# Performance work log

Hardware: AMD Instinct MI355X
Metric: run time of the kernel (lower is better)

## Reference

```python
import jax, jax.numpy as jnp
import numpy as np
from jax import lax

HORIZON = 333.0
LAM = 0.95
DISCOUNT = 1.0 - 1.0 / HORIZON  # contdisc=False

B, T, D, H = 1024, 65, 512, 512


def _mlp(x, W1, b1, W2, b2, W3, b3):
    # x: [B, T, D] -> scalar critic mean per step [B, T]
    h = jax.nn.silu(jnp.einsum('btd,dh->bth', x, W1) + b1)
    h = jax.nn.silu(jnp.einsum('bth,hk->btk', h, W2) + b2)
    out = jnp.einsum('bth,ho->bto', h, W3) + b3
    return out[..., 0]


def setup_inputs() -> dict:
    key = jax.random.key(0)
    ks = jax.random.split(key, 8)
    s = 1.0 / np.sqrt(D)
    sh = 1.0 / np.sqrt(H)
    return {
        'feat': jax.random.normal(ks[0], (B, T, D), jnp.float32),
        'reward': jax.random.normal(ks[1], (B, T), jnp.float32) * 0.1,
        'cont': jnp.ones((B, T), jnp.float32),
        'voffset': jnp.zeros((1,), jnp.float32),
        'vscale': jnp.ones((1,), jnp.float32),
        'W1n': jax.random.normal(ks[2], (D, H), jnp.float32) * s,
        'b1n': jnp.zeros((H,), jnp.float32),
        'W2n': jax.random.normal(ks[3], (H, H), jnp.float32) * sh,
        'b2n': jnp.zeros((H,), jnp.float32),
        'W3n': jax.random.normal(ks[4], (H, 1), jnp.float32) * sh,
        'b3n': jnp.zeros((1,), jnp.float32),
        'W1s': jax.random.normal(ks[5], (D, H), jnp.float32) * s,
        'b1s': jnp.zeros((H,), jnp.float32),
        'W2s': jax.random.normal(ks[6], (H, H), jnp.float32) * sh,
        'b2s': jnp.zeros((H,), jnp.float32),
        'W3s': jax.random.normal(ks[7], (H, 1), jnp.float32) * sh,
        'b3s': jnp.zeros((1,), jnp.float32),
    }


def reference(feat, reward, cont, voffset, vscale,
              W1n, b1n, W2n, b2n, W3n, b3n,
              W1s, b1s, W2s, b2s, W3s, b3s):
    critic = _mlp(feat, W1n, b1n, W2n, b2n, W3n, b3n)        # [B, T]
    slowcritic = _mlp(feat, W1s, b1s, W2s, b2s, W3s, b3s)    # [B, T]
    val = critic * vscale + voffset
    slowval = slowcritic * vscale + voffset
    tarval = slowval  # config.agent.slowtar = True

    disc = cont[:, 1:] * DISCOUNT                             # [B, T-1]
    interm = reward[:, 1:] + (1.0 - LAM) * disc * tarval[:, 1:]
    boot = tarval[:, -1]                                      # [B]

    # reversed linear recurrence r_t = interm_t + disc_t*lam*r_{t+1}
    xs = (jnp.moveaxis(interm, 1, 0), jnp.moveaxis(disc, 1, 0))  # [T-1, B]

    def step(carry, x):
        i_t, d_t = x
        r = i_t + d_t * LAM * carry
        return r, r

    _, ys = lax.scan(step, boot, xs, reverse=True)            # [T-1, B], time order t=0..T-2
    ret = jnp.moveaxis(ys, 0, 1)                              # [B, T-1]
    return ret
```

## Files before the change

### kernel.cpp

```cpp
#include <hip/hip_runtime.h>
#include <stdint.h>


#define MROWS 66560
#define RBLK 520
#define LAMF 0.95f
#define DISCF ((float)(1.0 - 1.0 / 333.0))

typedef __attribute__((ext_vector_type(8))) __bf16 bf16x8;
typedef __attribute__((ext_vector_type(4))) float f32x4;
typedef __attribute__((ext_vector_type(4))) unsigned int u32x4;

__device__ __forceinline__ unsigned short f2bf(float f) {
  unsigned int u = __float_as_uint(f);
  return (unsigned short)((u + 0x7FFFu + ((u >> 16) & 1u)) >> 16);
}
__device__ __forceinline__ float silu_f(float x) { return x / (1.0f + __expf(-x)); }

__device__ __forceinline__ void gload_lds16(const void* g, void* l) {
  __builtin_amdgcn_global_load_lds(
      (const __attribute__((address_space(1))) void*)g,
      (__attribute__((address_space(3))) void*)l, 16, 0, 0);
}

__device__ __forceinline__ u32x4 pack8(const f32x4& a, const f32x4& b) {
  union { unsigned short h[8]; u32x4 u; } p;
  p.h[0] = f2bf(a[0]); p.h[1] = f2bf(a[1]); p.h[2] = f2bf(a[2]); p.h[3] = f2bf(a[3]);
  p.h[4] = f2bf(b[0]); p.h[5] = f2bf(b[1]); p.h[6] = f2bf(b[2]); p.h[7] = f2bf(b[3]);
  return p.u;
}

__global__ __launch_bounds__(256) void prep_kernel(
    const float* __restrict__ W1, const float* __restrict__ W2,
    unsigned short* __restrict__ Wt1, unsigned short* __restrict__ Wt2,
    float* __restrict__ tarval) {
  int b = blockIdx.x;
  if (b < 128) {
    const float* W = (b < 64) ? W1 : W2;
    unsigned short* Wt = (b < 64) ? Wt1 : Wt2;
    int tb = b & 63;
    int tk = (tb >> 3) * 64;
    int tn = (tb & 7) * 64;
    __shared__ float tile[64][65];
    int tx = threadIdx.x & 63;
    int ty4 = threadIdx.x >> 6;
#pragma unroll
    for (int i = 0; i < 16; ++i) {
      int row = ty4 * 16 + i;
      tile[row][tx] = W[(size_t)(tk + row) * 512 + tn + tx];
    }
    __syncthreads();
#pragma unroll
    for (int i = 0; i < 16; ++i) {
      int nrow = ty4 * 16 + i;
      Wt[(size_t)(tn + nrow) * 512 + tk + tx] = f2bf(tile[tx][nrow]);
    }
  } else {
    int id = (b - 128) * 256 + threadIdx.x;
#pragma unroll
    for (int i = 0; i < 17; ++i) {
      int idx = id + i * 4096;
      if (idx < MROWS) tarval[idx] = 0.0f;
    }
  }
}

__device__ __forceinline__ void tile_map(int bid, int& rb, int& cb) {
  int xcd = bid & 7;
  int idx = bid >> 3;
  rb = xcd * 65 + (idx >> 2);
  cb = idx & 3;
}

__global__ __launch_bounds__(256) void gemm1_kernel(
    const float* __restrict__ A, const unsigned short* __restrict__ Bt,
    const float* __restrict__ bias, unsigned short* __restrict__ Hout) {
  __shared__ __align__(16) unsigned char lds[65536];

  int rb, cb; tile_map(blockIdx.x, rb, cb);
  const int m0 = rb * 128, n0 = cb * 128;
  const int tid = threadIdx.x;
  const int lane = tid & 63, w = tid >> 6;
  const int wr = w >> 1, wc = w & 1;
  const int q = lane >> 4, r = lane & 15;
  const unsigned int rx = (unsigned)(r & 7) << 4;

  f32x4 acc[4][4] = {};
  f32x4 pa[8];

  const int a_row_off = tid >> 3;
  const int a_col = (tid & 7) * 8;
  const unsigned int awx = ((unsigned)((tid >> 3) & 7)) << 4;
  const int b_row_off = w * 8 + (lane >> 3);
  const int b_col = ((lane & 7) ^ (lane >> 3)) * 8;

#pragma unroll
  for (int i = 0; i < 4; ++i) {
    const float* s = A + (size_t)(m0 + i * 32 + a_row_off) * 512 + a_col;
    pa[2 * i] = *(const f32x4*)s; pa[2 * i + 1] = *(const f32x4*)(s + 4);
  }
#pragma unroll
  for (int i = 0; i < 4; ++i)
    gload_lds16(Bt + (size_t)(n0 + i * 32 + b_row_off) * 512 + b_col,
                lds + 16384 + i * 4096 + w * 1024);
#pragma unroll
  for (int i = 0; i < 4; ++i)
    gload_lds16(Bt + (size_t)(n0 + i * 32 + b_row_off) * 512 + 64 + b_col,
                lds + 49152 + i * 4096 + w * 1024);
#pragma unroll
  for (int i = 0; i < 4; ++i)
    *(u32x4*)(lds + ((unsigned)(i * 4096 + tid * 16) ^ awx)) =
        pack8(pa[2 * i], pa[2 * i + 1]);

#pragma unroll
  for (int t = 0; t < 8; ++t) {
    if (t < 7) asm volatile("s_waitcnt vmcnt(4) lgkmcnt(0)" ::: "memory");
    else       asm volatile("s_waitcnt vmcnt(0) lgkmcnt(0)" ::: "memory");
    __builtin_amdgcn_s_barrier();

    unsigned char* Acur = lds + (t & 1) * 32768;
    unsigned char* Bcur = Acur + 16384;

    if (t < 7) {
      const int ks = (t + 1) * 64;
#pragma unroll
      for (int i = 0; i < 4; ++i) {
        const float* s = A + (size_t)(m0 + i * 32 + a_row_off) * 512 + ks + a_col;
        pa[2 * i] = *(const f32x4*)s; pa[2 * i + 1] = *(const f32x4*)(s + 4);
      }
    }

    bf16x8 af[2][4], bfr[2][4];
#pragma unroll
    for (int kk = 0; kk < 2; ++kk) {
      const unsigned int kb = kk * 64 + q * 16;
#pragma unroll
      for (int m = 0; m < 4; ++m) {
        const unsigned int row = wr * 64 + m * 16 + r;
        af[kk][m] = *(const bf16x8*)(Acur + ((row * 128 + kb) ^ rx));
      }
#pragma unroll
      for (int n = 0; n < 4; ++n) {
        const unsigned int row = wc * 64 + n * 16 + r;
        bfr[kk][n] = *(const bf16x8*)(Bcur + ((row * 128 + kb) ^ rx));
      }
    }
    asm volatile("s_waitcnt lgkmcnt(0)" ::: "memory");
    __builtin_amdgcn_sched_barrier(0);
    __builtin_amdgcn_s_barrier();

    if (t + 2 < 8) {
      const int ks = (t + 2) * 64;
#pragma unroll
      for (int i = 0; i < 4; ++i)
        gload_lds16(Bt + (size_t)(n0 + i * 32 + b_row_off) * 512 + ks + b_col,
                    Bcur + i * 4096 + w * 1024);
    }
    if (t < 7) {
      unsigned char* Anx = lds + ((t + 1) & 1) * 32768;
#pragma unroll
      for (int i = 0; i < 4; ++i)
        *(u32x4*)(Anx + ((unsigned)(i * 4096 + tid * 16) ^ awx)) =
            pack8(pa[2 * i], pa[2 * i + 1]);
    }

#pragma unroll
    for (int kk = 0; kk < 2; ++kk)
#pragma unroll
      for (int m = 0; m < 4; ++m)
#pragma unroll
        for (int n = 0; n < 4; ++n)
          acc[m][n] = __builtin_amdgcn_mfma_f32_16x16x32_bf16(af[kk][m], bfr[kk][n], acc[m][n], 0, 0, 0);
  }

#pragma unroll
  for (int n = 0; n < 4; ++n) {
    const int col = n0 + wc * 64 + n * 16 + r;
    const float bn = bias[col];
#pragma unroll
    for (int m = 0; m < 4; ++m) {
      const int rbase = m0 + wr * 64 + m * 16 + q * 4;
#pragma unroll
      for (int i = 0; i < 4; ++i)
        Hout[(size_t)(rbase + i) * 512 + col] = f2bf(silu_f(acc[m][n][i] + bn));
    }
  }
}

__global__ __launch_bounds__(256) void gemm2_kernel(
    const unsigned short* __restrict__ A, const unsigned short* __restrict__ Bt,
    const float* __restrict__ bias, const float* __restrict__ W3,
    float* __restrict__ tarval) {
  __shared__ __align__(16) unsigned char lds[65536];

  int rb, cb; tile_map(blockIdx.x, rb, cb);
  const int m0 = rb * 128, n0 = cb * 128;
  const int tid = threadIdx.x;
  const int lane = tid & 63, w = tid >> 6;
  const int wr = w >> 1, wc = w & 1;
  const int q = lane >> 4, r = lane & 15;
  const unsigned int rx = (unsigned)(r & 7) << 4;

  f32x4 acc[4][4] = {};
  const int s_row_off = w * 8 + (lane >> 3);
  const int s_col = ((lane & 7) ^ (lane >> 3)) * 8;

#pragma unroll
  for (int i = 0; i < 4; ++i) {
    gload_lds16(A  + (size_t)(m0 + i * 32 + s_row_off) * 512 + s_col,
                lds + i * 4096 + w * 1024);
    gload_lds16(Bt + (size_t)(n0 + i * 32 + s_row_off) * 512 + s_col,
                lds + 16384 + i * 4096 + w * 1024);
  }
#pragma unroll
  for (int i = 0; i < 4; ++i) {
    gload_lds16(A  + (size_t)(m0 + i * 32 + s_row_off) * 512 + 64 + s_col,
                lds + 32768 + i * 4096 + w * 1024);
    gload_lds16(Bt + (size_t)(n0 + i * 32 + s_row_off) * 512 + 64 + s_col,
                lds + 49152 + i * 4096 + w * 1024);
  }

#pragma unroll
  for (int t = 0; t < 8; ++t) {
    if (t < 7) asm volatile("s_waitcnt vmcnt(8) lgkmcnt(0)" ::: "memory");
    else       asm volatile("s_waitcnt vmcnt(0) lgkmcnt(0)" ::: "memory");
    __builtin_amdgcn_s_barrier();

    unsigned char* Acur = lds + (t & 1) * 32768;
    unsigned char* Bcur = Acur + 16384;

    bf16x8 af[2][4], bfr[2][4];
#pragma unroll
    for (int kk = 0; kk < 2; ++kk) {
      const unsigned int kb = kk * 64 + q * 16;
#pragma unroll
      for (int m = 0; m < 4; ++m) {
        const unsigned int row = wr * 64 + m * 16 + r;
        af[kk][m] = *(const bf16x8*)(Acur + ((row * 128 + kb) ^ rx));
      }
#pragma unroll
      for (int n = 0; n < 4; ++n) {
        const unsigned int row = wc * 64 + n * 16 + r;
        bfr[kk][n] = *(const bf16x8*)(Bcur + ((row * 128 + kb) ^ rx));
      }
    }
    asm volatile("s_waitcnt lgkmcnt(0)" ::: "memory");
    __builtin_amdgcn_sched_barrier(0);
    __builtin_amdgcn_s_barrier();

    if (t + 2 < 8) {
      const int ks = (t + 2) * 64;
#pragma unroll
      for (int i = 0; i < 4; ++i) {
        gload_lds16(A  + (size_t)(m0 + i * 32 + s_row_off) * 512 + ks + s_col,
                    Acur + i * 4096 + w * 1024);
        gload_lds16(Bt + (size_t)(n0 + i * 32 + s_row_off) * 512 + ks + s_col,
                    Bcur + i * 4096 + w * 1024);
      }
    }

#pragma unroll
    for (int kk = 0; kk < 2; ++kk)
#pragma unroll
      for (int m = 0; m < 4; ++m)
#pragma unroll
        for (int n = 0; n < 4; ++n)
          acc[m][n] = __builtin_amdgcn_mfma_f32_16x16x32_bf16(af[kk][m], bfr[kk][n], acc[m][n], 0, 0, 0);
  }

#pragma unroll
  for (int m = 0; m < 4; ++m) {
    float ps0 = 0.f, ps1 = 0.f, ps2 = 0.f, ps3 = 0.f;
#pragma unroll
    for (int n = 0; n < 4; ++n) {
      const int col = n0 + wc * 64 + n * 16 + r;
      const float bn = bias[col];
      const float w3 = W3[col];
      ps0 += silu_f(acc[m][n][0] + bn) * w3;
      ps1 += silu_f(acc[m][n][1] + bn) * w3;
      ps2 += silu_f(acc[m][n][2] + bn) * w3;
      ps3 += silu_f(acc[m][n][3] + bn) * w3;
    }
    float ps[4] = {ps0, ps1, ps2, ps3};
#pragma unroll
    for (int i = 0; i < 4; ++i) {
      float v = ps[i];
      v += __shfl_xor(v, 1);
      v += __shfl_xor(v, 2);
      v += __shfl_xor(v, 4);
      v += __shfl_xor(v, 8);
      if (r == 0) {
        int row = m0 + wr * 64 + m * 16 + q * 4 + i;
        atomicAdd(&tarval[row], v);
      }
    }
  }
}

__global__ __launch_bounds__(64) void scan_kernel(
    const float* __restrict__ tarval, const float* __restrict__ reward,
    const float* __restrict__ cont, const float* __restrict__ voffset,
    const float* __restrict__ vscale, const float* __restrict__ b3,
    float* __restrict__ out) {
  __shared__ float tv[64];
  __shared__ float ret[64];
  const int b = blockIdx.x, t = threadIdx.x;
  tv[t] = (tarval[b * 65 + 1 + t] + b3[0]) * vscale[0] + voffset[0];
  __syncthreads();
  if (t == 0) {
    float carry = tv[63];
    for (int j = 63; j >= 0; --j) {
      const int tt = j + 1;
      const float disc = cont[b * 65 + tt] * DISCF;
      const float r = reward[b * 65 + tt] + disc * ((1.0f - LAMF) * tv[j] + LAMF * carry);
      ret[j] = r;
      carry = r;
    }
  }
  __syncthreads();
  out[b * 64 + t] = ret[t];
}

extern "C" void kernel_launch(void* const* d_in, const int* in_sizes, int n_in,
                              void* d_out, int out_size, void* d_ws, size_t ws_size,
                              hipStream_t stream) {
  const float* feat    = (const float*)d_in[0];
  const float* reward  = (const float*)d_in[1];
  const float* cont    = (const float*)d_in[2];
  const float* voffset = (const float*)d_in[3];
  const float* vscale  = (const float*)d_in[4];
  const float* W1s = (const float*)d_in[11];
  const float* b1s = (const float*)d_in[12];
  const float* W2s = (const float*)d_in[13];
  const float* b2s = (const float*)d_in[14];
  const float* W3s = (const float*)d_in[15];
  const float* b3s = (const float*)d_in[16];

  char* ws = (char*)d_ws;
  unsigned short* Wt1 = (unsigned short*)ws;
  unsigned short* Wt2 = (unsigned short*)(ws + (512u << 10));
  float* tarval       = (float*)(ws + (1024u << 10));
  unsigned short* H1  = (unsigned short*)(ws + (2048u << 10));

  prep_kernel<<<144, 256, 0, stream>>>(W1s, W2s, Wt1, Wt2, tarval);
  gemm1_kernel<<<RBLK * 4, 256, 0, stream>>>(feat, Wt1, b1s, H1);
  gemm2_kernel<<<RBLK * 4, 256, 0, stream>>>(H1, Wt2, b2s, W3s, tarval);
  scan_kernel<<<1024, 64, 0, stream>>>(tarval, reward, cont, voffset, vscale, b3s,
                                       (float*)d_out);
}
```

Measured before the change: 343.0 us.

## Prefetch fp32 A two k-steps ahead, use native bf16 casts, parallel scan

In gemm1, the fp32 A-tile register prefetch now uses a two-stage register buffer and loads two k-steps ahead, with the vmcnt wait relaxed so more global loads stay in flight. Manual round-to-nearest bf16 packing is replaced with native __bf16 conversions, which may lower to hardware convert instructions. The serial single-thread reverse scan is replaced by a wavefront-parallel affine scan using shuffles, with four rows per block. In exchange, the extra A buffer raises register pressure, and the log-step scan changes floating-point summation order.

```diff
diff --git a/kernel.cpp b/kernel.cpp
--- a/kernel.cpp
+++ b/kernel.cpp
@@ -24,10 +24,15 @@
 }
 
 __device__ __forceinline__ u32x4 pack8(const f32x4& a, const f32x4& b) {
-  union { unsigned short h[8]; u32x4 u; } p;
-  p.h[0] = f2bf(a[0]); p.h[1] = f2bf(a[1]); p.h[2] = f2bf(a[2]); p.h[3] = f2bf(a[3]);
-  p.h[4] = f2bf(b[0]); p.h[5] = f2bf(b[1]); p.h[6] = f2bf(b[2]); p.h[7] = f2bf(b[3]);
+  union { __bf16 h[8]; u32x4 u; } p;
+  p.h[0] = (__bf16)a[0]; p.h[1] = (__bf16)a[1];
+  p.h[2] = (__bf16)a[2]; p.h[3] = (__bf16)a[3];
+  p.h[4] = (__bf16)b[0]; p.h[5] = (__bf16)b[1];
+  p.h[6] = (__bf16)b[2]; p.h[7] = (__bf16)b[3];
   return p.u;
+}
+__device__ __forceinline__ unsigned short f2bfc(float f) {
+  union { __bf16 h; unsigned short s; } u; u.h = (__bf16)f; return u.s;
 }
 
 __global__ __launch_bounds__(256) void prep_kernel(
@@ -86,7 +91,7 @@
   const unsigned int rx = (unsigned)(r & 7) << 4;
 
   f32x4 acc[4][4] = {};
-  f32x4 pa[8];
+  f32x4 pa[2][8];
 
   const int a_row_off = tid >> 3;
   const int a_col = (tid & 7) * 8;
@@ -97,36 +102,42 @@
 #pragma unroll
   for (int i = 0; i < 4; ++i) {
     const float* s = A + (size_t)(m0 + i * 32 + a_row_off) * 512 + a_col;
-    pa[2 * i] = *(const f32x4*)s; pa[2 * i + 1] = *(const f32x4*)(s + 4);
+    pa[0][2 * i] = *(const f32x4*)s; pa[0][2 * i + 1] = *(const f32x4*)(s + 4);
   }
 #pragma unroll
   for (int i = 0; i < 4; ++i)
     gload_lds16(Bt + (size_t)(n0 + i * 32 + b_row_off) * 512 + b_col,
                 lds + 16384 + i * 4096 + w * 1024);
 #pragma unroll
+  for (int i = 0; i < 4; ++i) {
+    const float* s = A + (size_t)(m0 + i * 32 + a_row_off) * 512 + 64 + a_col;
+    pa[1][2 * i] = *(const f32x4*)s; pa[1][2 * i + 1] = *(const f32x4*)(s + 4);
+  }
+#pragma unroll
   for (int i = 0; i < 4; ++i)
     gload_lds16(Bt + (size_t)(n0 + i * 32 + b_row_off) * 512 + 64 + b_col,
                 lds + 49152 + i * 4096 + w * 1024);
 #pragma unroll
   for (int i = 0; i < 4; ++i)
     *(u32x4*)(lds + ((unsigned)(i * 4096 + tid * 16) ^ awx)) =
-        pack8(pa[2 * i], pa[2 * i + 1]);
+        pack8(pa[0][2 * i], pa[0][2 * i + 1]);
 
 #pragma unroll
   for (int t = 0; t < 8; ++t) {
-    if (t < 7) asm volatile("s_waitcnt vmcnt(4) lgkmcnt(0)" ::: "memory");
+    if (t < 7) asm volatile("s_waitcnt vmcnt(8) lgkmcnt(0)" ::: "memory");
     else       asm volatile("s_waitcnt vmcnt(0) lgkmcnt(0)" ::: "memory");
     __builtin_amdgcn_s_barrier();
 
     unsigned char* Acur = lds + (t & 1) * 32768;
     unsigned char* Bcur = Acur + 16384;
 
-    if (t < 7) {
-      const int ks = (t + 1) * 64;
+    if (t + 2 < 8) {
+      const int ks = (t + 2) * 64;
 #pragma unroll
       for (int i = 0; i < 4; ++i) {
         const float* s = A + (size_t)(m0 + i * 32 + a_row_off) * 512 + ks + a_col;
-        pa[2 * i] = *(const f32x4*)s; pa[2 * i + 1] = *(const f32x4*)(s + 4);
+        pa[t & 1][2 * i] = *(const f32x4*)s;
+        pa[t & 1][2 * i + 1] = *(const f32x4*)(s + 4);
       }
     }
 
@@ -161,7 +172,7 @@
 #pragma unroll
       for (int i = 0; i < 4; ++i)
         *(u32x4*)(Anx + ((unsigned)(i * 4096 + tid * 16) ^ awx)) =
-            pack8(pa[2 * i], pa[2 * i + 1]);
+            pack8(pa[(t + 1) & 1][2 * i], pa[(t + 1) & 1][2 * i + 1]);
     }
 
 #pragma unroll
@@ -182,7 +193,7 @@
       const int rbase = m0 + wr * 64 + m * 16 + q * 4;
 #pragma unroll
       for (int i = 0; i < 4; ++i)
-        Hout[(size_t)(rbase + i) * 512 + col] = f2bf(silu_f(acc[m][n][i] + bn));
+        Hout[(size_t)(rbase + i) * 512 + col] = f2bfc(silu_f(acc[m][n][i] + bn));
     }
   }
 }
@@ -297,28 +308,27 @@
   }
 }
 
-__global__ __launch_bounds__(64) void scan_kernel(
+__global__ __launch_bounds__(256) void scan_kernel(
     const float* __restrict__ tarval, const float* __restrict__ reward,
     const float* __restrict__ cont, const float* __restrict__ voffset,
     const float* __restrict__ vscale, const float* __restrict__ b3,
     float* __restrict__ out) {
-  __shared__ float tv[64];
-  __shared__ float ret[64];
-  const int b = blockIdx.x, t = threadIdx.x;
-  tv[t] = (tarval[b * 65 + 1 + t] + b3[0]) * vscale[0] + voffset[0];
-  __syncthreads();
-  if (t == 0) {
-    float carry = tv[63];
-    for (int j = 63; j >= 0; --j) {
-      const int tt = j + 1;
-      const float disc = cont[b * 65 + tt] * DISCF;
-      const float r = reward[b * 65 + tt] + disc * ((1.0f - LAMF) * tv[j] + LAMF * carry);
-      ret[j] = r;
-      carry = r;
-    }
-  }
-  __syncthreads();
-  out[b * 64 + t] = ret[t];
+  const int row = blockIdx.x * 4 + (threadIdx.x >> 6);
+  const int t = threadIdx.x & 63;
+  const float vs = vscale[0], vo = voffset[0], bb = b3[0];
+  const int g = row * 65 + 1 + t;
+  const float tv = (tarval[g] + bb) * vs + vo;
+  const float dt = cont[g] * DISCF;
+  float ci = reward[g] + (1.0f - LAMF) * dt * tv;
+  float cc = dt * LAMF;
+  const float boot = __shfl(tv, 63, 64);
+#pragma unroll
+  for (int off = 1; off < 64; off <<= 1) {
+    float i2 = __shfl_down(ci, off, 64);
+    float c2 = __shfl_down(cc, off, 64);
+    if (t + off < 64) { ci = ci + cc * i2; cc = cc * c2; }
+  }
+  out[row * 64 + t] = ci + cc * boot;
 }
 
 extern "C" void kernel_launch(void* const* d_in, const int* in_sizes, int n_in,
@@ -345,6 +355,6 @@
   prep_kernel<<<144, 256, 0, stream>>>(W1s, W2s, Wt1, Wt2, tarval);
   gemm1_kernel<<<RBLK * 4, 256, 0, stream>>>(feat, Wt1, b1s, H1);
   gemm2_kernel<<<RBLK * 4, 256, 0, stream>>>(H1, Wt2, b2s, W3s, tarval);
-  scan_kernel<<<1024, 64, 0, stream>>>(tarval, reward, cont, voffset, vscale, b3s,
+  scan_kernel<<<256, 256, 0, stream>>>(tarval, reward, cont, voffset, vscale, b3s,
                                        (float*)d_out);
 }
```

Measured after the change: 361.6 us. 1.05x slower.
